# Performance work log

Hardware: AMD Instinct MI355X
Metric: run time of the kernel (lower is better)

Reference implementation:

```python
import jax, jax.numpy as jnp
import numpy as np

N = 100000   # nodes
E = 1600000  # edges (before self-loops)
IN, HID, OUT = 128, 16, 10
NEG_SLOPE = 0.2
LN_EPS = 1e-5


def layer_norm(x, gamma, beta):
    mu = jnp.mean(x, axis=-1, keepdims=True)
    var = jnp.mean((x - mu) ** 2, axis=-1, keepdims=True)
    return (x - mu) * jax.lax.rsqrt(var + LN_EPS) * gamma + beta


def gat_conv(x, edge_index, W, a_src, a_dst, bias, concat):
    # x: [N, Din], W: [Din, H*F], a_src/a_dst: [H, F]
    n = x.shape[0]
    H, F = a_src.shape
    h = (x @ W).reshape(n, H, F)                      # [N, H, F]
    src, dst = edge_index[0], edge_index[1]
    alpha_src = jnp.sum(h * a_src, axis=-1)           # [N, H]
    alpha_dst = jnp.sum(h * a_dst, axis=-1)           # [N, H]
    e = jax.nn.leaky_relu(alpha_src[src] + alpha_dst[dst], NEG_SLOPE)  # [E, H]
    # segment softmax over incoming edges of each dst node (self-loops guarantee non-empty)
    m = jax.ops.segment_max(e, dst, num_segments=n)
    e = jnp.exp(e - m[dst])
    s = jax.ops.segment_sum(e, dst, num_segments=n)
    alpha = e / (s[dst] + 1e-16)                      # [E, H]
    out = jax.ops.segment_sum(h[src] * alpha[:, :, None], dst, num_segments=n)  # [N, H, F]
    out = out.reshape(n, H * F) if concat else out.mean(axis=1)
    return out + bias


def setup_inputs() -> dict:
    key = jax.random.key(0)
    ks = jax.random.split(key, 20)
    d = {}
    d["x"] = jax.random.normal(ks[0], (N, IN), dtype=jnp.float32)
    d["edge_index"] = jax.random.randint(ks[1], (2, E), 0, N, dtype=jnp.int64)
    s = 0.1
    # layer 1: IN -> HID, 8 heads, concat
    d["W1"] = jax.random.normal(ks[2], (IN, 8 * HID), jnp.float32) * s
    d["a_src1"] = jax.random.normal(ks[3], (8, HID), jnp.float32) * s
    d["a_dst1"] = jax.random.normal(ks[4], (8, HID), jnp.float32) * s
    d["b1"] = jnp.zeros((8 * HID,), jnp.float32)
    d["g1"] = jnp.ones((8 * HID,), jnp.float32)
    d["be1"] = jnp.zeros((8 * HID,), jnp.float32)
    # layer 2: 8*HID -> HID, 4 heads, concat
    d["W2"] = jax.random.normal(ks[5], (8 * HID, 4 * HID), jnp.float32) * s
    d["a_src2"] = jax.random.normal(ks[6], (4, HID), jnp.float32) * s
    d["a_dst2"] = jax.random.normal(ks[7], (4, HID), jnp.float32) * s
    d["b2"] = jnp.zeros((4 * HID,), jnp.float32)
    d["g2"] = jnp.ones((4 * HID,), jnp.float32)
    d["be2"] = jnp.zeros((4 * HID,), jnp.float32)
    # layer 3: 4*HID -> OUT, 1 head, no concat
    d["W3"] = jax.random.normal(ks[8], (4 * HID, OUT), jnp.float32) * s
    d["a_src3"] = jax.random.normal(ks[9], (1, OUT), jnp.float32) * s
    d["a_dst3"] = jax.random.normal(ks[10], (1, OUT), jnp.float32) * s
    d["b3"] = jnp.zeros((OUT,), jnp.float32)
    return d


def reference(x, edge_index, W1, a_src1, a_dst1, b1, g1, be1,
              W2, a_src2, a_dst2, b2, g2, be2,
              W3, a_src3, a_dst3, b3):
    n = x.shape[0]
    loops = jnp.arange(n, dtype=edge_index.dtype)
    ei = jnp.concatenate([edge_index, jnp.stack([loops, loops])], axis=1)  # add self-loops
    h = gat_conv(x, ei, W1, a_src1, a_dst1, b1, concat=True)
    h = jax.nn.elu(layer_norm(h, g1, be1))
    h = gat_conv(h, ei, W2, a_src2, a_dst2, b2, concat=True)
    h = jax.nn.elu(layer_norm(h, g2, be2))
    h = gat_conv(h, ei, W3, a_src3, a_dst3, b3, concat=False)
    return jax.nn.log_softmax(h, axis=1)
```

## Files before the change

kernel.cpp:

```cpp
#include <hip/hip_runtime.h>
#include <hip/hip_bf16.h>
#include <math.h>

typedef __hip_bfloat16 bf16;
typedef __bf16 bf16x8 __attribute__((ext_vector_type(8)));
typedef float floatx4 __attribute__((ext_vector_type(4)));

__device__ __forceinline__ unsigned short f2bu(float f) {
    bf16 b = __float2bfloat16(f);
    return __builtin_bit_cast(unsigned short, b);
}
__device__ __forceinline__ float bu2f(unsigned short u) {
    return __uint_as_float(((unsigned)u) << 16);
}

template<int PF>
__device__ __forceinline__ void ldbfv(const unsigned short* p, float* v) {
    if constexpr (PF == 8) {
        uint4 u = *reinterpret_cast<const uint4*>(p);
        v[0] = __uint_as_float(u.x << 16); v[1] = __uint_as_float(u.x & 0xffff0000u);
        v[2] = __uint_as_float(u.y << 16); v[3] = __uint_as_float(u.y & 0xffff0000u);
        v[4] = __uint_as_float(u.z << 16); v[5] = __uint_as_float(u.z & 0xffff0000u);
        v[6] = __uint_as_float(u.w << 16); v[7] = __uint_as_float(u.w & 0xffff0000u);
    } else if constexpr (PF == 4) {
        uint2 u = *reinterpret_cast<const uint2*>(p);
        v[0] = __uint_as_float(u.x << 16); v[1] = __uint_as_float(u.x & 0xffff0000u);
        v[2] = __uint_as_float(u.y << 16); v[3] = __uint_as_float(u.y & 0xffff0000u);
    } else {
        unsigned u = *reinterpret_cast<const unsigned*>(p);
        v[0] = __uint_as_float(u << 16); v[1] = __uint_as_float(u & 0xffff0000u);
    }
}

template<typename XT, int H>
__global__ __launch_bounds__(256) void gemm_mfma(
    const XT* __restrict__ X, const float* __restrict__ W,
    const float* __restrict__ a_src, const float* __restrict__ a_dst,
    bf16* __restrict__ Hout, float* __restrict__ asrc, float* __restrict__ adst,
    int N)
{
    constexpr int M = H * 16;
    constexpr int KP = 136;
    constexpr int NT = M / 16;
    constexpr int HPQ = H / 4;
    __shared__ __align__(16) unsigned short Wt[M * KP];
    __shared__ __align__(16) unsigned short As[64 * KP];
    __shared__ float As_s[M], Ad_s[M];
    int tid = threadIdx.x;
    int r0 = blockIdx.x * 64;

    for (int i = tid; i < M; i += 256) { As_s[i] = a_src[i]; Ad_s[i] = a_dst[i]; }
    for (int idx = tid; idx < 128 * M; idx += 256) {
        int k = idx / M, m = idx % M;
        Wt[m * KP + k] = f2bu(W[idx]);
    }
    if constexpr (__is_same(XT, float)) {
        for (int idx = tid; idx < 64 * 32; idx += 256) {
            int row = idx >> 5, c4 = (idx & 31) * 4;
            int grow = r0 + row;
            float4 v = make_float4(0.f, 0.f, 0.f, 0.f);
            if (grow < N)
                v = *reinterpret_cast<const float4*>(X + (size_t)grow * 128 + c4);
            unsigned short* a = &As[row * KP + c4];
            a[0] = f2bu(v.x); a[1] = f2bu(v.y); a[2] = f2bu(v.z); a[3] = f2bu(v.w);
        }
    } else {
        for (int idx = tid; idx < 64 * 16; idx += 256) {
            int row = idx >> 4, c8 = (idx & 15) * 8;
            int grow = r0 + row;
            uint4 v = make_uint4(0u, 0u, 0u, 0u);
            if (grow < N)
                v = *reinterpret_cast<const uint4*>((const unsigned short*)X + (size_t)grow * 128 + c8);
            *reinterpret_cast<uint4*>(&As[row * KP + c8]) = v;
        }
    }
    __syncthreads();

    int w = tid >> 6, l = tid & 63, q = l >> 4, c = l & 15;
    floatx4 acc[NT];
    #pragma unroll
    for (int t = 0; t < NT; ++t) acc[t] = (floatx4){0.f, 0.f, 0.f, 0.f};

    #pragma unroll
    for (int kc = 0; kc < 4; ++kc) {
        bf16x8 a = *reinterpret_cast<const bf16x8*>(&As[(w * 16 + c) * KP + kc * 32 + q * 8]);
        #pragma unroll
        for (int t = 0; t < NT; ++t) {
            bf16x8 b = *reinterpret_cast<const bf16x8*>(&Wt[(t * 16 + c) * KP + kc * 32 + q * 8]);
            acc[t] = __builtin_amdgcn_mfma_f32_16x16x32_bf16(a, b, acc[t], 0, 0, 0);
        }
    }
    __syncthreads();
    #pragma unroll
    for (int t = 0; t < NT; ++t)
        #pragma unroll
        for (int r = 0; r < 4; ++r)
            As[(w * 16 + q * 4 + r) * KP + t * 16 + c] = f2bu(acc[t][r]);
    __syncthreads();
    for (int idx = tid; idx < 64 * (M / 8); idx += 256) {
        int row = idx / (M / 8), g = idx % (M / 8);
        int grow = r0 + row;
        if (grow < N)
            *reinterpret_cast<uint4*>(Hout + (size_t)grow * M + g * 8) =
                *reinterpret_cast<const uint4*>(&As[row * KP + g * 8]);
    }
    {
        int r = tid >> 2, qq = tid & 3;
        int grow = r0 + r;
        if (grow < N) {
            #pragma unroll
            for (int hh = 0; hh < HPQ; ++hh) {
                int hd = qq * HPQ + hh;
                float s1 = 0.f, s2 = 0.f;
                #pragma unroll
                for (int f = 0; f < 16; f += 2) {
                    unsigned u = *reinterpret_cast<const unsigned*>(&As[r * KP + hd * 16 + f]);
                    float v0 = __uint_as_float(u << 16);
                    float v1 = __uint_as_float(u & 0xffff0000u);
                    s1 += v0 * As_s[hd * 16 + f] + v1 * As_s[hd * 16 + f + 1];
                    s2 += v0 * Ad_s[hd * 16 + f] + v1 * Ad_s[hd * 16 + f + 1];
                }
                asrc[(size_t)grow * H + hd] = s1;
                adst[(size_t)grow * H + hd] = s2;
            }
        }
    }
}

#define CSR_CH  4096
#define CSR_REG 8192

__global__ __launch_bounds__(256) void csr_hist(
    const int* __restrict__ ei, int E, int DPB, int* __restrict__ histM)
{
    __shared__ int cnt[256];
    int tid = threadIdx.x;
    cnt[tid] = 0;
    __syncthreads();
    int e0 = blockIdx.x * CSR_CH;
    int e1 = min(E, e0 + CSR_CH);
    for (int e = e0 + tid; e < e1; e += 256)
        atomicAdd(&cnt[ei[E + e] / DPB], 1);
    __syncthreads();
    histM[blockIdx.x * 256 + tid] = cnt[tid];
}

__global__ __launch_bounds__(256) void csr_colscan(
    const int* __restrict__ histM, int NBLK,
    int* __restrict__ offT, int* __restrict__ btot)
{
    __shared__ int sm[512];
    int b = blockIdx.x;
    int tid = threadIdx.x;
    int i0 = tid, i1 = tid + 256;
    sm[i0] = (i0 < NBLK) ? histM[i0 * 256 + b] : 0;
    sm[i1] = (i1 < NBLK) ? histM[i1 * 256 + b] : 0;
    __syncthreads();
    #pragma unroll
    for (int o = 1; o < 512; o <<= 1) {
        int t0 = (i0 >= o) ? sm[i0 - o] : 0;
        int t1 = (i1 >= o) ? sm[i1 - o] : 0;
        __syncthreads();
        sm[i0] += t0; sm[i1] += t1;
        __syncthreads();
    }
    if (i0 < NBLK) offT[b * NBLK + i0] = b * CSR_REG + ((i0 == 0) ? 0 : sm[i0 - 1]);
    if (i1 < NBLK) offT[b * NBLK + i1] = b * CSR_REG + sm[i1 - 1];
    if (tid == 0) btot[b] = sm[511];
}

__global__ __launch_bounds__(256) void csr_pair_scatter(
    const int* __restrict__ ei, int E, int DPB,
    const int* __restrict__ offT, int NBLK,
    unsigned* __restrict__ pairs)
{
    __shared__ int cnt[256];
    int tid = threadIdx.x;
    int blk = blockIdx.x;
    cnt[tid] = offT[tid * NBLK + blk];
    __syncthreads();
    int e0 = blk * CSR_CH;
    int e1 = min(E, e0 + CSR_CH);
    for (int e = e0 + tid; e < e1; e += 256) {
        int s = ei[e];
        int d = ei[E + e];
        int b = d / DPB;
        int dloc = d - b * DPB;
        int pos = atomicAdd(&cnt[b], 1);
        pairs[pos] = ((unsigned)dloc << 17) | (unsigned)s;
    }
}

__global__ __launch_bounds__(256) void csr_fine(
    const unsigned* __restrict__ pairs, const int* __restrict__ btot,
    int DPB, int N, int2* __restrict__ ptrSE, int* __restrict__ col)
{
    __shared__ int sm[512];
    __shared__ int off[512];
    int b = blockIdx.x;
    int tid = threadIdx.x;
    int base = b * CSR_REG;
    int tot = btot[b];
    int d0 = b * DPB;
    int i0 = tid, i1 = tid + 256;
    sm[i0] = 0; sm[i1] = 0;
    __syncthreads();
    for (int i = tid; i < tot; i += 256)
        atomicAdd(&sm[pairs[base + i] >> 17], 1);
    __syncthreads();
    #pragma unroll
    for (int o = 1; o < 512; o <<= 1) {
        int t0 = (i0 >= o) ? sm[i0 - o] : 0;
        int t1 = (i1 >= o) ? sm[i1 - o] : 0;
        __syncthreads();
        sm[i0] += t0; sm[i1] += t1;
        __syncthreads();
    }
    int s0e = base + ((i0 == 0) ? 0 : sm[i0 - 1]);
    int s1e = base + sm[i1 - 1];
    off[i0] = s0e;
    off[i1] = s1e;
    if (i0 < DPB && d0 + i0 < N) ptrSE[d0 + i0] = make_int2(s0e, base + sm[i0]);
    if (i1 < DPB && d0 + i1 < N) ptrSE[d0 + i1] = make_int2(s1e, base + sm[i1]);
    __syncthreads();
    for (int i = tid; i < tot; i += 256) {
        unsigned p = pairs[base + i];
        int pos = atomicAdd(&off[p >> 17], 1);
        col[pos] = (int)(p & 0x1FFFFu);
    }
}

template<int M, int LPD>
__global__ __launch_bounds__(256) void agg_ln_kernel(
    const int2* __restrict__ ptrSE, const int* __restrict__ col,
    const float* __restrict__ asrc, const float* __restrict__ adst,
    const bf16* __restrict__ hb, const float* __restrict__ bias,
    const float* __restrict__ g, const float* __restrict__ be,
    bf16* __restrict__ out, int N)
{
    constexpr int PF = M / LPD;
    constexpr int H = M / 16;
    constexpr int DPBk = 256 / LPD;
    int tid = threadIdx.x;
    int sub = tid / LPD;
    int j = tid % LPD;
    int d = blockIdx.x * DPBk + sub;
    if (d >= N) return;
    int f0 = j * PF;
    int hd = f0 / 16;
    int2 se = ptrSE[d];
    int e = se.x, end = se.y;
    float adst_h = adst[d * H + hd];
    const unsigned short* hw = (const unsigned short*)hb;

    float ac0[PF], ac1[PF];
    float dn0, dn1 = 0.f;
    {
        float lg = asrc[d * H + hd] + adst_h;
        lg = lg > 0.f ? lg : 0.2f * lg;
        float w = __expf(lg);
        float v[PF];
        ldbfv<PF>(hw + (size_t)d * M + f0, v);
        #pragma unroll
        for (int p = 0; p < PF; ++p) { ac0[p] = w * v[p]; ac1[p] = 0.f; }
        dn0 = w;
    }
    for (; e + 4 <= end; e += 4) {
        int s0 = col[e], s1 = col[e + 1], s2 = col[e + 2], s3 = col[e + 3];
        float l0 = asrc[s0 * H + hd];
        float l1 = asrc[s1 * H + hd];
        float l2 = asrc[s2 * H + hd];
        float l3 = asrc[s3 * H + hd];
        float v0[PF], v1[PF], v2[PF], v3[PF];
        ldbfv<PF>(hw + (size_t)s0 * M + f0, v0);
        ldbfv<PF>(hw + (size_t)s1 * M + f0, v1);
        ldbfv<PF>(hw + (size_t)s2 * M + f0, v2);
        ldbfv<PF>(hw + (size_t)s3 * M + f0, v3);
        l0 += adst_h; l0 = l0 > 0.f ? l0 : 0.2f * l0; float w0 = __expf(l0);
        l1 += adst_h; l1 = l1 > 0.f ? l1 : 0.2f * l1; float w1 = __expf(l1);
        l2 += adst_h; l2 = l2 > 0.f ? l2 : 0.2f * l2; float w2 = __expf(l2);
        l3 += adst_h; l3 = l3 > 0.f ? l3 : 0.2f * l3; float w3 = __expf(l3);
        #pragma unroll
        for (int p = 0; p < PF; ++p) {
            ac0[p] += w0 * v0[p];
            ac1[p] += w1 * v1[p];
            ac0[p] += w2 * v2[p];
            ac1[p] += w3 * v3[p];
        }
        dn0 += w0 + w2; dn1 += w1 + w3;
    }
    for (; e < end; ++e) {
        int s = col[e];
        float lg = asrc[s * H + hd] + adst_h;
        lg = lg > 0.f ? lg : 0.2f * lg;
        float w = __expf(lg);
        float v[PF];
        ldbfv<PF>(hw + (size_t)s * M + f0, v);
        #pragma unroll
        for (int p = 0; p < PF; ++p) ac0[p] += w * v[p];
        dn0 += w;
    }

    float rden = 1.f / (dn0 + dn1 + 1e-16f);
    float o[PF];
    float sm1 = 0.f, sm2 = 0.f;
    #pragma unroll
    for (int p = 0; p < PF; ++p) {
        o[p] = (ac0[p] + ac1[p]) * rden + bias[f0 + p];
        sm1 += o[p];
        sm2 += o[p] * o[p];
    }
    #pragma unroll
    for (int off = LPD / 2; off >= 1; off >>= 1) {
        sm1 += __shfl_xor(sm1, off, LPD);
        sm2 += __shfl_xor(sm2, off, LPD);
    }
    float mu = sm1 * (1.f / M);
    float var = sm2 * (1.f / M) - mu * mu;
    float inv = rsqrtf(var + 1e-5f);
    unsigned pk[PF / 2];
    #pragma unroll
    for (int p = 0; p < PF; p += 2) {
        float y0 = (o[p] - mu) * inv * g[f0 + p] + be[f0 + p];
        float y1 = (o[p + 1] - mu) * inv * g[f0 + p + 1] + be[f0 + p + 1];
        y0 = y0 > 0.f ? y0 : expm1f(y0);
        y1 = y1 > 0.f ? y1 : expm1f(y1);
        pk[p / 2] = (unsigned)f2bu(y0) | ((unsigned)f2bu(y1) << 16);
    }
    unsigned short* op = (unsigned short*)out + (size_t)d * M + f0;
    if constexpr (PF == 8)
        *reinterpret_cast<uint4*>(op) = make_uint4(pk[0], pk[1], pk[2], pk[3]);
    else if constexpr (PF == 4)
        *reinterpret_cast<uint2*>(op) = make_uint2(pk[0], pk[1]);
    else
        *reinterpret_cast<unsigned*>(op) = pk[0];
}

__global__ __launch_bounds__(256) void gemm3_alpha(
    const bf16* __restrict__ X, const float* __restrict__ W3,
    const float* __restrict__ av_src, const float* __restrict__ av_dst,
    bf16* __restrict__ h3, float* __restrict__ asrc, float* __restrict__ adst,
    int N)
{
    __shared__ float Wl[640];
    int tid = threadIdx.x;
    for (int i = tid; i < 640; i += 256) Wl[i] = W3[i];
    __syncthreads();
    int n = blockIdx.x * 256 + tid;
    if (n >= N) return;
    float h[10];
    #pragma unroll
    for (int j = 0; j < 10; ++j) h[j] = 0.f;
    const unsigned short* xr = (const unsigned short*)X + (size_t)n * 64;
    for (int k2 = 0; k2 < 32; ++k2) {
        unsigned u = *reinterpret_cast<const unsigned*>(xr + k2 * 2);
        float x0 = __uint_as_float(u << 16);
        float x1 = __uint_as_float(u & 0xffff0000u);
        #pragma unroll
        for (int j = 0; j < 10; ++j)
            h[j] += x0 * Wl[(k2 * 2) * 10 + j] + x1 * Wl[(k2 * 2 + 1) * 10 + j];
    }
    float s1 = 0.f, s2 = 0.f;
    unsigned short* hr = (unsigned short*)h3 + (size_t)n * 16;
    #pragma unroll
    for (int j = 0; j < 10; j += 2) {
        unsigned u = (unsigned)f2bu(h[j]) | ((unsigned)f2bu(h[j + 1]) << 16);
        *reinterpret_cast<unsigned*>(hr + j) = u;
    }
    #pragma unroll
    for (int j = 0; j < 10; ++j) {
        s1 += h[j] * av_src[j];
        s2 += h[j] * av_dst[j];
    }
    asrc[n] = s1;
    adst[n] = s2;
}

__global__ __launch_bounds__(256) void agg_l3_final(
    const int2* __restrict__ ptrSE, const int* __restrict__ col,
    const float* __restrict__ asrc, const float* __restrict__ adst,
    const bf16* __restrict__ h, const float* __restrict__ b3,
    float* __restrict__ out, int N)
{
    int tid = threadIdx.x;
    int sub16 = tid >> 4;
    int j = tid & 15;
    int d = blockIdx.x * 16 + sub16;
    if (d >= N) return;
    const unsigned short* hu = (const unsigned short*)h;
    int2 se = ptrSE[d];
    int e = se.x, end = se.y;
    float adst_d = adst[d];
    float lg = asrc[d] + adst_d;
    lg = lg > 0.f ? lg : 0.2f * lg;
    float w = __expf(lg);
    bool act = j < 10;
    float a0 = act ? w * bu2f(hu[(size_t)d * 16 + j]) : 0.f;
    float a1 = 0.f, a2 = 0.f, a3 = 0.f;
    float d0 = w, d1 = 0.f, d2 = 0.f, d3 = 0.f;
    for (; e + 4 <= end; e += 4) {
        int s0 = col[e + 0], s1 = col[e + 1], s2 = col[e + 2], s3 = col[e + 3];
        float l0 = asrc[s0], l1 = asrc[s1], l2 = asrc[s2], l3 = asrc[s3];
        float v0 = act ? bu2f(hu[(size_t)s0 * 16 + j]) : 0.f;
        float v1 = act ? bu2f(hu[(size_t)s1 * 16 + j]) : 0.f;
        float v2 = act ? bu2f(hu[(size_t)s2 * 16 + j]) : 0.f;
        float v3 = act ? bu2f(hu[(size_t)s3 * 16 + j]) : 0.f;
        l0 += adst_d; l0 = l0 > 0.f ? l0 : 0.2f * l0; float w0 = __expf(l0);
        l1 += adst_d; l1 = l1 > 0.f ? l1 : 0.2f * l1; float w1 = __expf(l1);
        l2 += adst_d; l2 = l2 > 0.f ? l2 : 0.2f * l2; float w2 = __expf(l2);
        l3 += adst_d; l3 = l3 > 0.f ? l3 : 0.2f * l3; float w3 = __expf(l3);
        a0 += w0 * v0; a1 += w1 * v1; a2 += w2 * v2; a3 += w3 * v3;
        d0 += w0; d1 += w1; d2 += w2; d3 += w3;
    }
    for (; e < end; ++e) {
        int s = col[e];
        float l = asrc[s] + adst_d;
        l = l > 0.f ? l : 0.2f * l;
        float ww = __expf(l);
        if (act) a0 += ww * bu2f(hu[(size_t)s * 16 + j]);
        d0 += ww;
    }
    float den = d0 + d1 + d2 + d3;
    float v = (a0 + a1 + a2 + a3) / (den + 1e-16f);
    float lv = act ? v + b3[j] : -1e30f;
    float mx = lv;
    #pragma unroll
    for (int off = 1; off < 16; off <<= 1) mx = fmaxf(mx, __shfl_xor(mx, off, 16));
    float ev = act ? __expf(lv - mx) : 0.f;
    float se2 = ev;
    #pragma unroll
    for (int off = 1; off < 16; off <<= 1) se2 += __shfl_xor(se2, off, 16);
    float ls = mx + logf(se2);
    if (act) out[(size_t)d * 10 + j] = lv - ls;
}

static inline int cdiv(long a, long b) { return (int)((a + b - 1) / b); }

extern "C" void kernel_launch(void* const* d_in, const int* in_sizes, int n_in,
                              void* d_out, int out_size, void* d_ws, size_t ws_size,
                              hipStream_t stream)
{
    const float* x   = (const float*)d_in[0];
    const int*   ei  = (const int*)d_in[1];
    const float* W1  = (const float*)d_in[2];
    const float* as1 = (const float*)d_in[3];
    const float* ad1 = (const float*)d_in[4];
    const float* b1  = (const float*)d_in[5];
    const float* g1  = (const float*)d_in[6];
    const float* be1 = (const float*)d_in[7];
    const float* W2  = (const float*)d_in[8];
    const float* as2 = (const float*)d_in[9];
    const float* ad2 = (const float*)d_in[10];
    const float* b2  = (const float*)d_in[11];
    const float* g2  = (const float*)d_in[12];
    const float* be2 = (const float*)d_in[13];
    const float* W3  = (const float*)d_in[14];
    const float* as3 = (const float*)d_in[15];
    const float* ad3 = (const float*)d_in[16];
    const float* b3  = (const float*)d_in[17];

    const int N = in_sizes[0] / 128;
    const int E = in_sizes[1] / 2;

    const int DPB  = cdiv(N, 256);
    const int NBLK = cdiv(E, CSR_CH);

    bf16*     hb    = (bf16*)d_ws;
    bf16*     aggb  = hb + (size_t)N * 128;
    float*    asrc  = (float*)(aggb + (size_t)N * 128);
    float*    adst  = asrc + (size_t)N * 8;
    unsigned* pairs = (unsigned*)(adst + (size_t)N * 8);
    int*      col   = (int*)(pairs + 256 * CSR_REG);
    int2*     ptrSE = (int2*)(col + 256 * CSR_REG);
    int*      histM = (int*)(ptrSE + N);
    int*      offT  = histM + (size_t)NBLK * 256;
    int*      btot  = offT + (size_t)NBLK * 256;
    bf16*     h3b   = hb;

    csr_hist<<<NBLK, 256, 0, stream>>>(ei, E, DPB, histM);
    csr_colscan<<<256, 256, 0, stream>>>(histM, NBLK, offT, btot);
    csr_pair_scatter<<<NBLK, 256, 0, stream>>>(ei, E, DPB, offT, NBLK, pairs);
    csr_fine<<<256, 256, 0, stream>>>(pairs, btot, DPB, N, ptrSE, col);

    gemm_mfma<float, 8><<<cdiv(N, 64), 256, 0, stream>>>(x, W1, as1, ad1, hb, asrc, adst, N);
    agg_ln_kernel<128, 16><<<cdiv(N, 16), 256, 0, stream>>>(ptrSE, col, asrc, adst, hb, b1, g1, be1, aggb, N);

    gemm_mfma<bf16, 4><<<cdiv(N, 64), 256, 0, stream>>>(aggb, W2, as2, ad2, hb, asrc, adst, N);
    agg_ln_kernel<64, 16><<<cdiv(N, 16), 256, 0, stream>>>(ptrSE, col, asrc, adst, hb, b2, g2, be2, aggb, N);

    gemm3_alpha<<<cdiv(N, 256), 256, 0, stream>>>(aggb, W3, as3, ad3, h3b, asrc, adst, N);
    agg_l3_final<<<cdiv(N, 16), 256, 0, stream>>>(ptrSE, col, asrc, adst, h3b, b3, (float*)d_out, N);
}
```

Before: 378.5 us.

## Fuse CSR histogram into layer-1 GEMM and fold layer-3 projection into layer-2 aggregation

The CSR histogram blocks are appended to the layer-1 MFMA GEMM launch, so both run concurrently in one kernel and one launch is removed. The layer-2 aggregation+LayerNorm+ELU kernel now also computes the 64x10 layer-3 projection and its attention logits with a 16-lane shuffle reduction. This removes the separate gemm3 kernel and the write and re-read of the layer-2 output. In exchange it adds shuffle work per node and a slightly different workspace layout, with separate asrc3/adst3 buffers and h3 stored in aggb.

Result: no change. 375.9 us (-0.7%).

```diff
diff --git a/kernel.cpp b/kernel.cpp
--- a/kernel.cpp
+++ b/kernel.cpp
@@ -5,6 +5,9 @@
 typedef __hip_bfloat16 bf16;
 typedef __bf16 bf16x8 __attribute__((ext_vector_type(8)));
 typedef float floatx4 __attribute__((ext_vector_type(4)));
+
+#define CSR_CH  4096
+#define CSR_REG 8192
 
 __device__ __forceinline__ unsigned short f2bu(float f) {
     bf16 b = __float2bfloat16(f);
@@ -37,7 +40,8 @@
     const XT* __restrict__ X, const float* __restrict__ W,
     const float* __restrict__ a_src, const float* __restrict__ a_dst,
     bf16* __restrict__ Hout, float* __restrict__ asrc, float* __restrict__ adst,
-    int N)
+    int N, int NG, const int* __restrict__ ei, int E, int DPB,
+    int* __restrict__ histM)
 {
     constexpr int M = H * 16;
     constexpr int KP = 136;
@@ -47,8 +51,22 @@
     __shared__ __align__(16) unsigned short As[64 * KP];
     __shared__ float As_s[M], Ad_s[M];
     int tid = threadIdx.x;
+
+    if (blockIdx.x >= NG) {
+        int* cnt = (int*)Wt;
+        cnt[tid] = 0;
+        __syncthreads();
+        int blk = blockIdx.x - NG;
+        int e0 = blk * CSR_CH;
+        int e1 = min(E, e0 + CSR_CH);
+        for (int e = e0 + tid; e < e1; e += 256)
+            atomicAdd(&cnt[ei[E + e] / DPB], 1);
+        __syncthreads();
+        histM[blk * 256 + tid] = cnt[tid];
+        return;
+    }
+
     int r0 = blockIdx.x * 64;
-
     for (int i = tid; i < M; i += 256) { As_s[i] = a_src[i]; Ad_s[i] = a_dst[i]; }
     for (int idx = tid; idx < 128 * M; idx += 256) {
         int k = idx / M, m = idx % M;
@@ -127,24 +145,6 @@
     }
 }
 
-#define CSR_CH  4096
-#define CSR_REG 8192
-
-__global__ __launch_bounds__(256) void csr_hist(
-    const int* __restrict__ ei, int E, int DPB, int* __restrict__ histM)
-{
-    __shared__ int cnt[256];
-    int tid = threadIdx.x;
-    cnt[tid] = 0;
-    __syncthreads();
-    int e0 = blockIdx.x * CSR_CH;
-    int e1 = min(E, e0 + CSR_CH);
-    for (int e = e0 + tid; e < e1; e += 256)
-        atomicAdd(&cnt[ei[E + e] / DPB], 1);
-    __syncthreads();
-    histM[blockIdx.x * 256 + tid] = cnt[tid];
-}
-
 __global__ __launch_bounds__(256) void csr_colscan(
     const int* __restrict__ histM, int NBLK,
     int* __restrict__ offT, int* __restrict__ btot)
@@ -336,44 +336,130 @@
         *reinterpret_cast<unsigned*>(op) = pk[0];
 }
 
-__global__ __launch_bounds__(256) void gemm3_alpha(
-    const bf16* __restrict__ X, const float* __restrict__ W3,
-    const float* __restrict__ av_src, const float* __restrict__ av_dst,
-    bf16* __restrict__ h3, float* __restrict__ asrc, float* __restrict__ adst,
+__global__ __launch_bounds__(256) void agg_ln_l2_g3(
+    const int2* __restrict__ ptrSE, const int* __restrict__ col,
+    const float* __restrict__ asrc, const float* __restrict__ adst,
+    const bf16* __restrict__ hb, const float* __restrict__ bias,
+    const float* __restrict__ g, const float* __restrict__ be,
+    const float* __restrict__ W3, const float* __restrict__ as3,
+    const float* __restrict__ ad3,
+    bf16* __restrict__ h3, float* __restrict__ asrc3, float* __restrict__ adst3,
     int N)
 {
-    __shared__ float Wl[640];
+    constexpr int M = 64, LPD = 16, PF = 4, H = 4, DPBk = 16;
+    __shared__ float Wl[640], s3[10], d3[10];
     int tid = threadIdx.x;
     for (int i = tid; i < 640; i += 256) Wl[i] = W3[i];
-    __syncthreads();
-    int n = blockIdx.x * 256 + tid;
-    if (n >= N) return;
-    float h[10];
-    #pragma unroll
-    for (int j = 0; j < 10; ++j) h[j] = 0.f;
-    const unsigned short* xr = (const unsigned short*)X + (size_t)n * 64;
-    for (int k2 = 0; k2 < 32; ++k2) {
-        unsigned u = *reinterpret_cast<const unsigned*>(xr + k2 * 2);
-        float x0 = __uint_as_float(u << 16);
-        float x1 = __uint_as_float(u & 0xffff0000u);
-        #pragma unroll
-        for (int j = 0; j < 10; ++j)
-            h[j] += x0 * Wl[(k2 * 2) * 10 + j] + x1 * Wl[(k2 * 2 + 1) * 10 + j];
-    }
-    float s1 = 0.f, s2 = 0.f;
-    unsigned short* hr = (unsigned short*)h3 + (size_t)n * 16;
-    #pragma unroll
-    for (int j = 0; j < 10; j += 2) {
-        unsigned u = (unsigned)f2bu(h[j]) | ((unsigned)f2bu(h[j + 1]) << 16);
-        *reinterpret_cast<unsigned*>(hr + j) = u;
-    }
-    #pragma unroll
-    for (int j = 0; j < 10; ++j) {
-        s1 += h[j] * av_src[j];
-        s2 += h[j] * av_dst[j];
-    }
-    asrc[n] = s1;
-    adst[n] = s2;
+    if (tid < 10) { s3[tid] = as3[tid]; d3[tid] = ad3[tid]; }
+    __syncthreads();
+    int sub = tid >> 4;
+    int j = tid & 15;
+    int d = blockIdx.x * DPBk + sub;
+    if (d >= N) return;
+    int f0 = j * PF;
+    int hd = f0 / 16;
+    int2 se = ptrSE[d];
+    int e = se.x, end = se.y;
+    float adst_h = adst[d * H + hd];
+    const unsigned short* hw = (const unsigned short*)hb;
+
+    float ac0[PF], ac1[PF];
+    float dn0, dn1 = 0.f;
+    {
+        float lg = asrc[d * H + hd] + adst_h;
+        lg = lg > 0.f ? lg : 0.2f * lg;
+        float w = __expf(lg);
+        float v[PF];
+        ldbfv<PF>(hw + (size_t)d * M + f0, v);
+        #pragma unroll
+        for (int p = 0; p < PF; ++p) { ac0[p] = w * v[p]; ac1[p] = 0.f; }
+        dn0 = w;
+    }
+    for (; e + 4 <= end; e += 4) {
+        int s0 = col[e], s1 = col[e + 1], s2 = col[e + 2], s3i = col[e + 3];
+        float l0 = asrc[s0 * H + hd];
+        float l1 = asrc[s1 * H + hd];
+        float l2 = asrc[s2 * H + hd];
+        float l3 = asrc[s3i * H + hd];
+        float v0[PF], v1[PF], v2[PF], v3[PF];
+        ldbfv<PF>(hw + (size_t)s0 * M + f0, v0);
+        ldbfv<PF>(hw + (size_t)s1 * M + f0, v1);
+        ldbfv<PF>(hw + (size_t)s2 * M + f0, v2);
+        ldbfv<PF>(hw + (size_t)s3i * M + f0, v3);
+        l0 += adst_h; l0 = l0 > 0.f ? l0 : 0.2f * l0; float w0 = __expf(l0);
+        l1 += adst_h; l1 = l1 > 0.f ? l1 : 0.2f * l1; float w1 = __expf(l1);
+        l2 += adst_h; l2 = l2 > 0.f ? l2 : 0.2f * l2; float w2 = __expf(l2);
+        l3 += adst_h; l3 = l3 > 0.f ? l3 : 0.2f * l3; float w3 = __expf(l3);
+        #pragma unroll
+        for (int p = 0; p < PF; ++p) {
+            ac0[p] += w0 * v0[p];
+            ac1[p] += w1 * v1[p];
+            ac0[p] += w2 * v2[p];
+            ac1[p] += w3 * v3[p];
+        }
+        dn0 += w0 + w2; dn1 += w1 + w3;
+    }
+    for (; e < end; ++e) {
+        int s = col[e];
+        float lg = asrc[s * H + hd] + adst_h;
+        lg = lg > 0.f ? lg : 0.2f * lg;
+        float w = __expf(lg);
+        float v[PF];
+        ldbfv<PF>(hw + (size_t)s * M + f0, v);
+        #pragma unroll
+        for (int p = 0; p < PF; ++p) ac0[p] += w * v[p];
+        dn0 += w;
+    }
+
+    float rden = 1.f / (dn0 + dn1 + 1e-16f);
+    float o[PF];
+    float sm1 = 0.f, sm2 = 0.f;
+    #pragma unroll
+    for (int p = 0; p < PF; ++p) {
+        o[p] = (ac0[p] + ac1[p]) * rden + bias[f0 + p];
+        sm1 += o[p];
+        sm2 += o[p] * o[p];
+    }
+    #pragma unroll
+    for (int off = 8; off >= 1; off >>= 1) {
+        sm1 += __shfl_xor(sm1, off, 16);
+        sm2 += __shfl_xor(sm2, off, 16);
+    }
+    float mu = sm1 * (1.f / M);
+    float var = sm2 * (1.f / M) - mu * mu;
+    float inv = rsqrtf(var + 1e-5f);
+    float y[PF];
+    #pragma unroll
+    for (int p = 0; p < PF; ++p) {
+        float t = (o[p] - mu) * inv * g[f0 + p] + be[f0 + p];
+        y[p] = t > 0.f ? t : expm1f(t);
+    }
+    float pj[10];
+    #pragma unroll
+    for (int jj = 0; jj < 10; ++jj)
+        pj[jj] = y[0] * Wl[(f0 + 0) * 10 + jj] + y[1] * Wl[(f0 + 1) * 10 + jj]
+               + y[2] * Wl[(f0 + 2) * 10 + jj] + y[3] * Wl[(f0 + 3) * 10 + jj];
+    #pragma unroll
+    for (int off = 8; off >= 1; off >>= 1)
+        #pragma unroll
+        for (int jj = 0; jj < 10; ++jj)
+            pj[jj] += __shfl_xor(pj[jj], off, 16);
+    if (j == 0) {
+        unsigned short* hr = (unsigned short*)h3 + (size_t)d * 16;
+        #pragma unroll
+        for (int jj = 0; jj < 10; jj += 2) {
+            unsigned u = (unsigned)f2bu(pj[jj]) | ((unsigned)f2bu(pj[jj + 1]) << 16);
+            *reinterpret_cast<unsigned*>(hr + jj) = u;
+        }
+        float a1 = 0.f, a2 = 0.f;
+        #pragma unroll
+        for (int jj = 0; jj < 10; ++jj) {
+            a1 += pj[jj] * s3[jj];
+            a2 += pj[jj] * d3[jj];
+        }
+        asrc3[d] = a1;
+        adst3[d] = a2;
+    }
 }
 
 __global__ __launch_bounds__(256) void agg_l3_final(
@@ -469,25 +555,35 @@
     bf16*     aggb  = hb + (size_t)N * 128;
     float*    asrc  = (float*)(aggb + (size_t)N * 128);
     float*    adst  = asrc + (size_t)N * 8;
-    unsigned* pairs = (unsigned*)(adst + (size_t)N * 8);
+    float*    asrc3 = adst + (size_t)N * 8;
+    float*    adst3 = asrc3 + N;
+    unsigned* pairs = (unsigned*)(adst3 + N);
     int*      col   = (int*)(pairs + 256 * CSR_REG);
     int2*     ptrSE = (int2*)(col + 256 * CSR_REG);
     int*      histM = (int*)(ptrSE + N);
     int*      offT  = histM + (size_t)NBLK * 256;
     int*      btot  = offT + (size_t)NBLK * 256;
-    bf16*     h3b   = hb;
-
-    csr_hist<<<NBLK, 256, 0, stream>>>(ei, E, DPB, histM);
+    bf16*     h3b   = aggb;
+
+    const int NG1 = cdiv(N, 64);
+
+    gemm_mfma<float, 8><<<NG1 + NBLK, 256, 0, stream>>>(
+        x, W1, as1, ad1, hb, asrc, adst, N, NG1, ei, E, DPB, histM);
     csr_colscan<<<256, 256, 0, stream>>>(histM, NBLK, offT, btot);
     csr_pair_scatter<<<NBLK, 256, 0, stream>>>(ei, E, DPB, offT, NBLK, pairs);
     csr_fine<<<256, 256, 0, stream>>>(pairs, btot, DPB, N, ptrSE, col);
 
-    gemm_mfma<float, 8><<<cdiv(N, 64), 256, 0, stream>>>(x, W1, as1, ad1, hb, asrc, adst, N);
-    agg_ln_kernel<128, 16><<<cdiv(N, 16), 256, 0, stream>>>(ptrSE, col, asrc, adst, hb, b1, g1, be1, aggb, N);
-
-    gemm_mfma<bf16, 4><<<cdiv(N, 64), 256, 0, stream>>>(aggb, W2, as2, ad2, hb, asrc, adst, N);
-    agg_ln_kernel<64, 16><<<cdiv(N, 16), 256, 0, stream>>>(ptrSE, col, asrc, adst, hb, b2, g2, be2, aggb, N);
-
-    gemm3_alpha<<<cdiv(N, 256), 256, 0, stream>>>(aggb, W3, as3, ad3, h3b, asrc, adst, N);
-    agg_l3_final<<<cdiv(N, 16), 256, 0, stream>>>(ptrSE, col, asrc, adst, h3b, b3, (float*)d_out, N);
-}
+    agg_ln_kernel<128, 16><<<cdiv(N, 16), 256, 0, stream>>>(
+        ptrSE, col, asrc, adst, hb, b1, g1, be1, aggb, N);
+
+    const int NG2 = cdiv(N, 64);
+    gemm_mfma<bf16, 4><<<NG2, 256, 0, stream>>>(
+        aggb, W2, as2, ad2, hb, asrc, adst, N, NG2, nullptr, 0, 1, nullptr);
+
+    agg_ln_l2_g3<<<cdiv(N, 16), 256, 0, stream>>>(
+        ptrSE, col, asrc, adst, hb, b2, g2, be2, W3, as3, ad3,
+        h3b, asrc3, adst3, N);
+
+    agg_l3_final<<<cdiv(N, 16), 256, 0, stream>>>(
+        ptrSE, col, asrc3, adst3, h3b, b3, (float*)d_out, N);
+}
```
